# Kernel optimization log

Hardware: AMD Instinct MI355X
Metric: run time of the kernel (lower is better)

The kernel has to match this reference:

```python
import jax, jax.numpy as jnp
import numpy as np

# Module config (matches init_kwargs)
N_HEADS = 16
HEAD = 64
SEQ = 4096          # single prefill sequence (cu_seqlens_k = [0, SEQ])
BS = 64             # block_size (both q and k blocks)
LOCAL = 8           # local_blocks
VERT = 8            # vert_stride
NB = SEQ // BS      # number of blocks along seq
SLIDE = max(1, VERT // N_HEADS)  # get_head_sliding_step(16, 8, homo_head=False) -> 1
SM_SCALE = 1.0 / float(np.sqrt(HEAD))


def _build_layout():
    """Per-head block-sparse layout: causal + (local OR strided-vertical) blocks,
    padded to a fixed max nnz per row (CSR rows -> padded col indices + valid mask)."""
    h = np.arange(N_HEADS)[:, None, None]
    i = np.arange(NB)[None, :, None]
    j = np.arange(NB)[None, None, :]
    mask = (j <= i) & (((i - j) < LOCAL) | (((j + h * SLIDE + 1) % VERT) == 0))
    max_nnz = int(mask.sum(-1).max())
    cols = np.zeros((N_HEADS, NB, max_nnz), np.int32)
    valid = np.zeros((N_HEADS, NB, max_nnz), bool)
    for hh in range(N_HEADS):
        for ii in range(NB):
            c = np.nonzero(mask[hh, ii])[0]
            cols[hh, ii, :len(c)] = c
            valid[hh, ii, :len(c)] = True
    return cols, valid, max_nnz

_COLS_NP, _VALID_NP, MAX_NNZ = _build_layout()
COLS = jnp.asarray(_COLS_NP)    # [H, NB, NNZ] k-block ids (padded with 0)
VALID = jnp.asarray(_VALID_NP)  # [H, NB, NNZ] padding mask


def setup_inputs() -> dict:
    key = jax.random.key(0)
    kq, kk, kv = jax.random.split(key, 3)
    q = jax.random.normal(kq, (SEQ, N_HEADS, HEAD), jnp.float32)
    k = jax.random.normal(kk, (SEQ, N_HEADS, HEAD), jnp.float32)
    v = jax.random.normal(kv, (SEQ, N_HEADS, HEAD), jnp.float32)
    cu_seqlens_k = jnp.array([0, SEQ], jnp.int32)
    return {"q": q, "k": k, "v": v, "cu_seqlens_k": cu_seqlens_k}


def _attn(q, k, v):
    # [T, H, D] -> [H, NB, BS, D]
    qb = q.transpose(1, 0, 2).reshape(N_HEADS, NB, BS, HEAD)
    kb = k.transpose(1, 0, 2).reshape(N_HEADS, NB, BS, HEAD)
    vb = v.transpose(1, 0, 2).reshape(N_HEADS, NB, BS, HEAD)
    gather = jax.vmap(lambda x, c: x[c])  # per-head block gather
    kg = gather(kb, COLS)  # [H, NB, NNZ, BS, D]
    vg = gather(vb, COLS)  # [H, NB, NNZ, BS, D]
    # block-sparse scores: [H, NB(q blk), BS(m), NNZ(n), BS(j)]
    scores = jnp.einsum('himd,hinjd->himnj', qb, kg) * SM_SCALE
    qpos = jnp.arange(NB)[:, None] * BS + jnp.arange(BS)[None, :]   # [NB, BS]
    kpos = COLS[..., None] * BS + jnp.arange(BS)                    # [H, NB, NNZ, BS]
    allow = VALID[:, :, None, :, None] & (
        qpos[None, :, :, None, None] >= kpos[:, :, None, :, :])
    scores = jnp.where(allow, scores, -jnp.inf)
    p = jax.nn.softmax(scores.reshape(N_HEADS, NB, BS, MAX_NNZ * BS), axis=-1)
    p = p.reshape(N_HEADS, NB, BS, MAX_NNZ, BS)
    out = jnp.einsum('himnj,hinjd->himd', p, vg)
    return out.reshape(N_HEADS, SEQ, HEAD).transpose(1, 0, 2)  # [T, H, D]


def reference(q, k, v, cu_seqlens_k):
    # single-sequence prefill: past_len = 0, q_len == k_len == SEQ
    return _attn(q, k, v)
```

## Files before the change

### kernel.cpp

```cpp
#include <hip/hip_runtime.h>
#include <hip/hip_bf16.h>
#include <math.h>


#define NHEADS 16
#define HDIM   64
#define NBLK   64
#define SEQLEN 4096
#define KP     72
#define SMAX   16.0f

typedef __attribute__((ext_vector_type(8))) short bf16x8;
typedef __attribute__((ext_vector_type(4))) float f32x4;

__device__ __forceinline__ short f2bf(float x) {
    union { float f; unsigned u; } c; c.f = x;
    unsigned u = c.u;
    return (short)((u + 0x7FFFu + ((u >> 16) & 1u)) >> 16);
}
__device__ __forceinline__ short f2bf_trunc(float x) {
    union { float f; unsigned u; } c; c.f = x;
    return (short)(c.u >> 16);
}

__device__ __forceinline__ void load_lds16(const short* g, const short* l) {
    __builtin_amdgcn_global_load_lds(
        (const __attribute__((address_space(1))) void*)g,
        (__attribute__((address_space(3))) void*)l, 16, 0, 0);
}

__global__ __launch_bounds__(256)
void prep_kernel(const float* __restrict__ k, const float* __restrict__ v,
                 short* __restrict__ kt, short* __restrict__ vt) {
    __shared__ short tile[64 * KP];
    const int b = blockIdx.x;
    const int h = b >> 6, jb = b & 63;
    const int tid = threadIdx.x;

    #pragma unroll
    for (int it = 0; it < 4; ++it) {
        int e = it * 1024 + tid * 4;
        int key = e >> 6, d0 = e & 63;
        float4 f = *(const float4*)(v + ((size_t)(jb * 64 + key) * NHEADS + h) * HDIM + d0);
        tile[(d0 + 0) * KP + key] = f2bf(f.x);
        tile[(d0 + 1) * KP + key] = f2bf(f.y);
        tile[(d0 + 2) * KP + key] = f2bf(f.z);
        tile[(d0 + 3) * KP + key] = f2bf(f.w);
    }
    __syncthreads();
    short* vtile = vt + (size_t)b * 4096;
    #pragma unroll
    for (int ii = 0; ii < 2; ++ii) {
        int idx = ii * 256 + tid;
        int d = idx >> 3, gsw = idx & 7;
        int g = gsw ^ (d & 7);
        bf16x8 val = *(const bf16x8*)&tile[d * KP + g * 8];
        *(bf16x8*)(vtile + (size_t)idx * 8) = val;
    }
    short* ktile = kt + (size_t)b * 4096;
    #pragma unroll
    for (int ii = 0; ii < 2; ++ii) {
        int idx = ii * 256 + tid;
        int r = idx >> 3, g = idx & 7;
        const float* src = k + ((size_t)(jb * 64 + r) * NHEADS + h) * HDIM + g * 8;
        float4 f0 = *(const float4*)src;
        float4 f1 = *(const float4*)(src + 4);
        bf16x8 a;
        a[0]=f2bf(f0.x); a[1]=f2bf(f0.y); a[2]=f2bf(f0.z); a[3]=f2bf(f0.w);
        a[4]=f2bf(f1.x); a[5]=f2bf(f1.y); a[6]=f2bf(f1.z); a[7]=f2bf(f1.w);
        int G = r * 8 + (g ^ (r & 7));
        *(bf16x8*)(ktile + (size_t)G * 8) = a;
    }
}

__global__ __launch_bounds__(512, 4)
void attn_kernel(const short* __restrict__ kt, const short* __restrict__ vt,
                 const float* __restrict__ q, float* __restrict__ out) {
    __shared__ short kv[2 * 8192];
    __shared__ short pl[8 * 1024];

    const int b    = blockIdx.x;
    const int h    = ((b & 7) << 1) | ((b >> 3) & 1);
    const int g5   = b >> 4;
    const int m    = (g5 < 16) ? g5 : (47 - g5);
    const int q0   = 2 * m, q1 = 2 * m + 1;
    const int tid  = threadIdx.x;
    const int wave = tid >> 6;
    const int lane = tid & 63;
    const int l16  = lane & 15;
    const int quad = lane >> 4;

    const int myqi   = q0 + (wave >> 2);
    const int stripe = wave & 3;
    const int row0   = myqi * 64 + stripe * 16;
    short* pw = pl + wave * 1024;

    const float* qrow = q + ((size_t)(row0 + l16) * NHEADS + h) * HDIM;
    bf16x8 a_q[2];
    #pragma unroll
    for (int kk = 0; kk < 2; ++kk) {
        const float* src = qrow + kk * 32 + quad * 8;
        float4 f0 = *(const float4*)(src);
        float4 f1 = *(const float4*)(src + 4);
        bf16x8 a;
        a[0]=f2bf(f0.x); a[1]=f2bf(f0.y); a[2]=f2bf(f0.z); a[3]=f2bf(f0.w);
        a[4]=f2bf(f1.x); a[5]=f2bf(f1.y); a[6]=f2bf(f1.z); a[7]=f2bf(f1.w);
        a_q[kk] = a;
    }

    f32x4 o[4];
    float lsum[4];
    #pragma unroll
    for (int nt = 0; nt < 4; ++nt) { o[nt] = (f32x4){0.f,0.f,0.f,0.f}; lsum[nt] = 0.f; }

    const short* kth = kt + (size_t)(h * 64) * 4096;
    const short* vth = vt + (size_t)(h * 64) * 4096;
    const float kscale = 0.125f * 1.4426950408889634f;

    const int j0  = (7 - h) & 7;
    const int l0  = (q0 > 7) ? (q0 - 7) : 0;
    const int nv  = (j0 < l0) ? ((l0 - j0 + 7) >> 3) : 0;
    const int T   = nv + (q1 - l0 + 1);

    const int r7   = l16 & 7;
    const int gk0  = (quad ^ r7) * 8;
    const int gk1  = gk0 ^ 32;
    const int rowb = l16 * 64;
    const int pr0  = rowb + (((  quad) ^ r7) << 3);
    const int pr1  = rowb + (((4 + quad) ^ r7) << 3);

    {
        const short* ktb = kth + (size_t)((0 < nv) ? j0 : l0) * 4096;
        const short* vtb = vth + (size_t)((0 < nv) ? j0 : l0) * 4096;
        load_lds16(ktb + (size_t)tid * 8, &kv[wave * 512]);
        load_lds16(vtb + (size_t)tid * 8, &kv[4096 + wave * 512]);
    }

    for (int t = 0; t < T; ++t) {
        const int jb = (t < nv) ? (j0 + 8 * t) : (l0 + (t - nv));

        __syncthreads();

        if (t + 1 < T) {
            const int jn = (t + 1 < nv) ? (j0 + 8 * (t + 1)) : (l0 + (t + 1 - nv));
            const int bo = ((t + 1) & 1) * 8192;
            const short* ktb = kth + (size_t)jn * 4096;
            const short* vtb = vth + (size_t)jn * 4096;
            load_lds16(ktb + (size_t)tid * 8, &kv[bo + wave * 512]);
            load_lds16(vtb + (size_t)tid * 8, &kv[bo + 4096 + wave * 512]);
        }

        const bool part = (jb <= myqi) &&
                          (((myqi - jb) < 8) || (((jb + h + 1) & 7) == 0));
        if (part) {
            const short* kb = &kv[(t & 1) * 8192];
            const short* vb = kb + 4096;

            f32x4 s[4];
            #pragma unroll
            for (int nt = 0; nt < 4; ++nt) {
                bf16x8 k0 = *(const bf16x8*)&kb[nt * 1024 + rowb + gk0];
                bf16x8 k1 = *(const bf16x8*)&kb[nt * 1024 + rowb + gk1];
                s[nt] = (f32x4){0.f,0.f,0.f,0.f};
                s[nt] = __builtin_amdgcn_mfma_f32_16x16x32_bf16(a_q[0], k0, s[nt], 0, 0, 0);
                s[nt] = __builtin_amdgcn_mfma_f32_16x16x32_bf16(a_q[1], k1, s[nt], 0, 0, 0);
            }

            const bool diag = (jb == myqi);
            #pragma unroll
            for (int nt = 0; nt < 4; ++nt) {
                const int gw = nt * 2 + (l16 >> 3);
                const int ow = l16 & 7;
                #pragma unroll
                for (int r = 0; r < 4; ++r) {
                    float raw = s[nt][r];
                    const int mrow = stripe * 16 + quad * 4 + r;
                    if (diag) {
                        int n = nt * 16 + l16;
                        if (n > mrow) raw = -INFINITY;
                    }
                    float pv = __builtin_amdgcn_exp2f(fmaf(raw, kscale, -SMAX));
                    lsum[r] += pv;
                    const int prow = quad * 4 + r;
                    pw[prow * 64 + ((gw ^ (prow & 7)) << 3) + ow] = f2bf_trunc(pv);
                }
            }

            bf16x8 a_p0 = *(const bf16x8*)&pw[pr0];
            bf16x8 a_p1 = *(const bf16x8*)&pw[pr1];

            #pragma unroll
            for (int nt = 0; nt < 4; ++nt) {
                bf16x8 v0 = *(const bf16x8*)&vb[nt * 1024 + rowb + gk0];
                bf16x8 v1 = *(const bf16x8*)&vb[nt * 1024 + rowb + gk1];
                o[nt] = __builtin_amdgcn_mfma_f32_16x16x32_bf16(a_p0, v0, o[nt], 0, 0, 0);
                o[nt] = __builtin_amdgcn_mfma_f32_16x16x32_bf16(a_p1, v1, o[nt], 0, 0, 0);
            }
        }
    }

    #pragma unroll
    for (int r = 0; r < 4; ++r) {
        float tsum = lsum[r];
        #pragma unroll
        for (int off = 1; off < 16; off <<= 1)
            tsum += __shfl_xor(tsum, off);
        float inv = 1.0f / tsum;
        int trow = row0 + quad * 4 + r;
        float* orow = out + ((size_t)trow * NHEADS + h) * HDIM;
        #pragma unroll
        for (int nt = 0; nt < 4; ++nt)
            orow[nt * 16 + l16] = o[nt][r] * inv;
    }
}

extern "C" void kernel_launch(void* const* d_in, const int* in_sizes, int n_in,
                              void* d_out, int out_size, void* d_ws, size_t ws_size,
                              hipStream_t stream) {
    const float* q = (const float*)d_in[0];
    const float* k = (const float*)d_in[1];
    const float* v = (const float*)d_in[2];
    float* out = (float*)d_out;

    const size_t tileBytes = (size_t)NHEADS * NBLK * 4096 * sizeof(short);
    short* kt = (short*)d_ws;
    short* vt = (short*)((char*)d_ws + tileBytes);
    prep_kernel<<<dim3(NHEADS * NBLK), dim3(256), 0, stream>>>(k, v, kt, vt);
    attn_kernel<<<dim3(512), dim3(512), 0, stream>>>(kt, vt, q, out);
}
```

Measured before the change: 119.3 us.

## Compute transposed scores so P stays in registers, dropping LDS round-trip

```diff
diff --git a/kernel.cpp b/kernel.cpp
--- a/kernel.cpp
+++ b/kernel.cpp
@@ -9,6 +9,7 @@
 #define SEQLEN 4096
 #define KP     72
 #define SMAX   16.0f
+#define NEGBIG (-1.0e30f)
 
 typedef __attribute__((ext_vector_type(8))) short bf16x8;
 typedef __attribute__((ext_vector_type(4))) float f32x4;
@@ -27,6 +28,11 @@
     __builtin_amdgcn_global_load_lds(
         (const __attribute__((address_space(1))) void*)g,
         (__attribute__((address_space(3))) void*)l, 16, 0, 0);
+}
+
+__device__ __forceinline__ void drain_then_sync() {
+    asm volatile("s_waitcnt vmcnt(0)" ::: "memory");
+    __syncthreads();
 }
 
 __global__ __launch_bounds__(256)
@@ -54,7 +60,13 @@
         int idx = ii * 256 + tid;
         int d = idx >> 3, gsw = idx & 7;
         int g = gsw ^ (d & 7);
-        bf16x8 val = *(const bf16x8*)&tile[d * KP + g * 8];
+        bf16x8 val;
+        #pragma unroll
+        for (int j = 0; j < 8; ++j) {
+            int s   = g * 8 + j;
+            int key = (s & 32) | (((s >> 2) & 1) << 4) | (((s >> 3) & 3) << 2) | (s & 3);
+            val[j]  = tile[d * KP + key];
+        }
         *(bf16x8*)(vtile + (size_t)idx * 8) = val;
     }
     short* ktile = kt + (size_t)b * 4096;
@@ -77,7 +89,6 @@
 void attn_kernel(const short* __restrict__ kt, const short* __restrict__ vt,
                  const float* __restrict__ q, float* __restrict__ out) {
     __shared__ short kv[2 * 8192];
-    __shared__ short pl[8 * 1024];
 
     const int b    = blockIdx.x;
     const int h    = ((b & 7) << 1) | ((b >> 3) & 1);
@@ -93,7 +104,6 @@
     const int myqi   = q0 + (wave >> 2);
     const int stripe = wave & 3;
     const int row0   = myqi * 64 + stripe * 16;
-    short* pw = pl + wave * 1024;
 
     const float* qrow = q + ((size_t)(row0 + l16) * NHEADS + h) * HDIM;
     bf16x8 a_q[2];
@@ -109,9 +119,9 @@
     }
 
     f32x4 o[4];
-    float lsum[4];
-    #pragma unroll
-    for (int nt = 0; nt < 4; ++nt) { o[nt] = (f32x4){0.f,0.f,0.f,0.f}; lsum[nt] = 0.f; }
+    #pragma unroll
+    for (int nt = 0; nt < 4; ++nt) o[nt] = (f32x4){0.f,0.f,0.f,0.f};
+    float lsum = 0.f;
 
     const short* kth = kt + (size_t)(h * 64) * 4096;
     const short* vth = vt + (size_t)(h * 64) * 4096;
@@ -126,8 +136,7 @@
     const int gk0  = (quad ^ r7) * 8;
     const int gk1  = gk0 ^ 32;
     const int rowb = l16 * 64;
-    const int pr0  = rowb + (((  quad) ^ r7) << 3);
-    const int pr1  = rowb + (((4 + quad) ^ r7) << 3);
+    const int qrl  = stripe * 16 + l16;
 
     {
         const short* ktb = kth + (size_t)((0 < nv) ? j0 : l0) * 4096;
@@ -139,7 +148,7 @@
     for (int t = 0; t < T; ++t) {
         const int jb = (t < nv) ? (j0 + 8 * t) : (l0 + (t - nv));
 
-        __syncthreads();
+        drain_then_sync();
 
         if (t + 1 < T) {
             const int jn = (t + 1 < nv) ? (j0 + 8 * (t + 1)) : (l0 + (t + 1 - nv));
@@ -155,39 +164,38 @@
         if (part) {
             const short* kb = &kv[(t & 1) * 8192];
             const short* vb = kb + 4096;
+            const bool diag = (jb == myqi);
 
             f32x4 s[4];
             #pragma unroll
             for (int nt = 0; nt < 4; ++nt) {
                 bf16x8 k0 = *(const bf16x8*)&kb[nt * 1024 + rowb + gk0];
                 bf16x8 k1 = *(const bf16x8*)&kb[nt * 1024 + rowb + gk1];
-                s[nt] = (f32x4){0.f,0.f,0.f,0.f};
-                s[nt] = __builtin_amdgcn_mfma_f32_16x16x32_bf16(a_q[0], k0, s[nt], 0, 0, 0);
-                s[nt] = __builtin_amdgcn_mfma_f32_16x16x32_bf16(a_q[1], k1, s[nt], 0, 0, 0);
+                f32x4 acc = (f32x4){0.f, 0.f, 0.f, 0.f};
+                acc = __builtin_amdgcn_mfma_f32_16x16x32_bf16(k0, a_q[0], acc, 0, 0, 0);
+                acc = __builtin_amdgcn_mfma_f32_16x16x32_bf16(k1, a_q[1], acc, 0, 0, 0);
+                s[nt] = acc;
             }
 
-            const bool diag = (jb == myqi);
+            short pb[4][4];
             #pragma unroll
             for (int nt = 0; nt < 4; ++nt) {
-                const int gw = nt * 2 + (l16 >> 3);
-                const int ow = l16 & 7;
                 #pragma unroll
                 for (int r = 0; r < 4; ++r) {
+                    const int keyl = nt * 16 + quad * 4 + r;
                     float raw = s[nt][r];
-                    const int mrow = stripe * 16 + quad * 4 + r;
-                    if (diag) {
-                        int n = nt * 16 + l16;
-                        if (n > mrow) raw = -INFINITY;
-                    }
+                    raw = (diag && (keyl > qrl)) ? NEGBIG : raw;
                     float pv = __builtin_amdgcn_exp2f(fmaf(raw, kscale, -SMAX));
-                    lsum[r] += pv;
-                    const int prow = quad * 4 + r;
-                    pw[prow * 64 + ((gw ^ (prow & 7)) << 3) + ow] = f2bf_trunc(pv);
+                    lsum += pv;
+                    pb[nt][r] = f2bf_trunc(pv);
                 }
             }
 
-            bf16x8 a_p0 = *(const bf16x8*)&pw[pr0];
-            bf16x8 a_p1 = *(const bf16x8*)&pw[pr1];
+            bf16x8 a_p0, a_p1;
+            a_p0[0]=pb[0][0]; a_p0[1]=pb[0][1]; a_p0[2]=pb[0][2]; a_p0[3]=pb[0][3];
+            a_p0[4]=pb[1][0]; a_p0[5]=pb[1][1]; a_p0[6]=pb[1][2]; a_p0[7]=pb[1][3];
+            a_p1[0]=pb[2][0]; a_p1[1]=pb[2][1]; a_p1[2]=pb[2][2]; a_p1[3]=pb[2][3];
+            a_p1[4]=pb[3][0]; a_p1[5]=pb[3][1]; a_p1[6]=pb[3][2]; a_p1[7]=pb[3][3];
 
             #pragma unroll
             for (int nt = 0; nt < 4; ++nt) {
@@ -199,18 +207,18 @@
         }
     }
 
+    float tsum = lsum;
+    tsum += __shfl_xor(tsum, 16);
+    tsum += __shfl_xor(tsum, 32);
+    const float inv = 1.0f / tsum;
     #pragma unroll
     for (int r = 0; r < 4; ++r) {
-        float tsum = lsum[r];
-        #pragma unroll
-        for (int off = 1; off < 16; off <<= 1)
-            tsum += __shfl_xor(tsum, off);
-        float inv = 1.0f / tsum;
+        float invr = __shfl(inv, quad * 4 + r);
         int trow = row0 + quad * 4 + r;
         float* orow = out + ((size_t)trow * NHEADS + h) * HDIM;
         #pragma unroll
         for (int nt = 0; nt < 4; ++nt)
-            orow[nt * 16 + l16] = o[nt][r] * inv;
+            orow[nt * 16 + l16] = o[nt][r] * invr;
     }
 }
 
```

Result: faster. 114.6 us (-4.0%).
